# Kernel tuning notes

Hardware: AMD Instinct MI355X
Metric: run time of the kernel (lower is better)

## Reference

```python
import jax, jax.numpy as jnp
import numpy as np


def setup_inputs() -> dict:
    key = jax.random.key(0)
    kq, kk, kv = jax.random.split(key, 3)
    B, L, S, H, E = 2, 2048, 2048, 8, 64
    queries = jax.random.normal(kq, (B, L, H, E), dtype=jnp.float32)
    keys = jax.random.normal(kk, (B, S, H, E), dtype=jnp.float32)
    values = jax.random.normal(kv, (B, S, H, E), dtype=jnp.float32)
    a1 = jnp.float32(1.0)
    a2 = jnp.float32(1.0)
    return {"queries": queries, "keys": keys, "values": values, "a1": a1, "a2": a2}


def reference(queries, keys, values, a1, a2):
    # queries: (B,L,H,E); keys/values: (B,S,H,E)
    E = queries.shape[-1]
    scale = 1.0 / jnp.sqrt(jnp.float32(E))
    # shared QK scores: (B,H,L,S)
    qk = jnp.einsum('blhe,bshe->bhls', queries, keys) * scale
    # sparse branch: relu^2 (dropout = identity in eval)
    ssa = jnp.square(jax.nn.relu(qk))
    ssa_out = jnp.einsum('bhls,bshd->blhd', ssa, values)
    # dense branch: softmax over keys
    dsa = jax.nn.softmax(qk, axis=-1)
    dsa_out = jnp.einsum('bhls,bshd->blhd', dsa, values)
    w1 = jnp.exp(a1)
    w2 = jnp.exp(a2)
    alpha1 = w1 / (w1 + w2)
    alpha2 = w2 / (w1 + w2)
    return alpha1 * ssa_out + alpha2 * dsa_out
```

## Files before the change

kernel.cpp:

```cpp
#include <hip/hip_runtime.h>

typedef short short4v __attribute__((ext_vector_type(4)));
typedef short short8v __attribute__((ext_vector_type(8)));
typedef float float4v __attribute__((ext_vector_type(4)));
typedef unsigned short u16;

#define NB 2
#define NL 2048
#define NS 2048
#define NH 8
#define NE 64
#define HE (NH*NE)
#define NLT (NL/64)
#define NST (NS/64)
#define TILE_U16 4096

static __device__ __forceinline__ unsigned pk2bf(float a, float b) {
  union { float f; unsigned u; } x, y; x.f = a; y.f = b;
  return __builtin_amdgcn_perm(y.u + 0x8000u, x.u + 0x8000u, 0x07060302u);
}

static __device__ __forceinline__ unsigned cvtpk(float a, float b) {
  unsigned r;
  asm("v_cvt_pk_bf16_f32 %0, %1, %2" : "=v"(r) : "v"(a), "v"(b));
  return r;
}

static __device__ __forceinline__ float fexp2(float x) {
  float r;
  asm("v_exp_f32 %0, %1" : "=v"(r) : "v"(x));
  return r;
}

#define GLD16(gp, lp) __builtin_amdgcn_global_load_lds( \
    (const __attribute__((address_space(1))) void*)(gp), \
    (__attribute__((address_space(3))) void*)(lp), 16, 0, 0)

static __device__ __forceinline__ int fK(int s) { return (s & 3) | ((s >> 1) & 4); }

__global__ __launch_bounds__(256)
void prepack(const float* __restrict__ kp, const float* __restrict__ vp,
             u16* __restrict__ kimg, u16* __restrict__ vimg)
{
  __shared__ __align__(16) u16 ldsv[TILE_U16];

  const int bid  = blockIdx.x;
  const int tile = bid >> 1;
  const int doV  = bid & 1;
  const int st = tile & (NST - 1);
  const int bh = tile >> 5;
  const int h  = bh & (NH - 1);
  const int b  = bh >> 3;
  const int s0 = st * 64;
  const size_t base = (size_t)b * NS * HE + h * NE;
  const int tid  = threadIdx.x;
  const int wv   = tid >> 6;
  const int lane = tid & 63;
  const int ln7  = lane & 7;

  if (!doV) {
    u16* kt = kimg + (size_t)tile * TILE_U16;
    for (int slot = tid; slot < 512; slot += 256) {
      const int srow = slot >> 3, p = slot & 7, c = p ^ fK(srow);
      const float* src = kp + base + (size_t)(s0 + srow) * HE + c * 8;
      float4 x0 = *(const float4*)src;
      float4 x1 = *(const float4*)(src + 4);
      unsigned d[4] = { pk2bf(x0.x, x0.y), pk2bf(x0.z, x0.w),
                        pk2bf(x1.x, x1.y), pk2bf(x1.z, x1.w) };
      *(int4*)(kt + slot * 8) = *(const int4*)d;
    }
    return;
  }

  u16* vt = vimg + (size_t)tile * TILE_U16;
  {
    const float* vcol = vp + base + (size_t)(s0 + wv * 16) * HE + lane;
    unsigned vr[8];
    #pragma unroll
    for (int jj = 0; jj < 8; ++jj)
      vr[jj] = pk2bf(vcol[(size_t)(2 * jj) * HE], vcol[(size_t)(2 * jj + 1) * HE]);
    #pragma unroll
    for (int i = 0; i < 2; ++i) {
      const int cs = (2 * wv + i) ^ ln7;
      int4 t4 = make_int4((int)vr[4*i+0], (int)vr[4*i+1],
                          (int)vr[4*i+2], (int)vr[4*i+3]);
      *(int4*)(&ldsv[lane * 64 + cs * 8]) = t4;
    }
  }
  __syncthreads();
  {
    const int4* s = (const int4*)ldsv;
    int4* dst = (int4*)vt;
    dst[tid]       = s[tid];
    dst[tid + 256] = s[tid + 256];
  }
}

__global__ __launch_bounds__(512, 2)
void assa_fwd(const float* __restrict__ qp, const u16* __restrict__ kimg,
              const u16* __restrict__ vimg, const float* __restrict__ a1p,
              const float* __restrict__ a2p, float* __restrict__ op)
{
  __shared__ __align__(16) u16 ldsb[2][2][2 * TILE_U16];

  const int tid  = threadIdx.x;
  const int wv   = tid >> 6;
  const int ws   = wv & 3;
  const int strm = wv >> 2;
  const int lane = tid & 63;
  const int ln15 = lane & 15;
  const int ln7  = lane & 7;
  const int quad = lane >> 4;

  const int bid = blockIdx.x;
  const int bh  = bid & 15;
  const int lt  = bid >> 4;
  const int h   = bh & (NH - 1);
  const int b   = bh >> 3;

  const int lbase = lt * 64 + ws * 16;

  short8v qf0, qf1;
  {
    const float qs = 0.125f * 1.44269504089f;
    const float* qrow = qp + ((size_t)(b * NL + lbase + ln15)) * HE + h * NE + quad * 8;
    float4 q0 = *(const float4*)(qrow);
    float4 q1 = *(const float4*)(qrow + 4);
    float4 q2 = *(const float4*)(qrow + 32);
    float4 q3 = *(const float4*)(qrow + 36);
    unsigned d0[4] = { pk2bf(qs*q0.x, qs*q0.y), pk2bf(qs*q0.z, qs*q0.w),
                       pk2bf(qs*q1.x, qs*q1.y), pk2bf(qs*q1.z, qs*q1.w) };
    unsigned d1[4] = { pk2bf(qs*q2.x, qs*q2.y), pk2bf(qs*q2.z, qs*q2.w),
                       pk2bf(qs*q3.x, qs*q3.y), pk2bf(qs*q3.z, qs*q3.w) };
    qf0 = *(const short8v*)d0;
    qf1 = *(const short8v*)d1;
  }

  short8v ones8;
  #pragma unroll
  for (int j = 0; j < 8; ++j) ones8[j] = (short)0x3F80;

  const size_t tbase = (size_t)bh * NST;

  float4v acc_s[4], acc_d[4], acc_l;
  #pragma unroll
  for (int t = 0; t < 4; ++t)
    #pragma unroll
    for (int r = 0; r < 4; ++r) { acc_s[t][r] = 0.0f; acc_d[t][r] = 0.0f; }
  #pragma unroll
  for (int r = 0; r < 4; ++r) acc_l[r] = 0.0f;

  auto dma_tile = [&](int st, int nb) {
    const int hf = ws & 1;
    const u16* g;
    u16* l;
    if (ws < 2) {
      g = kimg + (tbase + st) * TILE_U16 + hf * 2048 + lane * 8;
      l = &ldsb[strm][nb][hf * 2048];
    } else {
      g = vimg + (tbase + st) * TILE_U16 + hf * 2048 + lane * 8;
      l = &ldsb[strm][nb][TILE_U16 + hf * 2048];
    }
    GLD16(g,        l);
    GLD16(g +  512, l +  512);
    GLD16(g + 1024, l + 1024);
    GLD16(g + 1536, l + 1536);
  };

  dma_tile(strm, 0);

  const int rperm = 8 * (ln15 >> 2) + (ln15 & 3);
  const int fk    = (ln15 & 3) | (((ln15 >> 2) & 1) << 2);

  for (int it = 0; it < NST / 2; ++it) {
    asm volatile("s_waitcnt vmcnt(0)" ::: "memory");
    __builtin_amdgcn_s_barrier();
    asm volatile("" ::: "memory");
    if (it + 1 < NST / 2) dma_tile(2 * (it + 1) + strm, (it + 1) & 1);

    const u16* kb_l = ldsb[strm][it & 1];
    const u16* vb_l = kb_l + TILE_U16;

    #pragma unroll
    for (int U = 0; U < 2; ++U) {
      float4v sa0, sa1;
      #pragma unroll
      for (int r = 0; r < 4; ++r) { sa0[r] = 0.0f; sa1[r] = 0.0f; }
      const u16* krow0 = &kb_l[(32 * U + rperm) * 64];
      const u16* krow1 = krow0 + 4 * 64;
      short8v kf00 = *(const short8v*)(krow0 + (quad ^ fk) * 8);
      short8v kf01 = *(const short8v*)(krow0 + ((4 + quad) ^ fk) * 8);
      short8v kf10 = *(const short8v*)(krow1 + (quad ^ fk) * 8);
      short8v kf11 = *(const short8v*)(krow1 + ((4 + quad) ^ fk) * 8);
      __builtin_amdgcn_s_setprio(1);
      sa0 = __builtin_amdgcn_mfma_f32_16x16x32_bf16(kf00, qf0, sa0, 0, 0, 0);
      sa0 = __builtin_amdgcn_mfma_f32_16x16x32_bf16(kf01, qf1, sa0, 0, 0, 0);
      sa1 = __builtin_amdgcn_mfma_f32_16x16x32_bf16(kf10, qf0, sa1, 0, 0, 0);
      sa1 = __builtin_amdgcn_mfma_f32_16x16x32_bf16(kf11, qf1, sa1, 0, 0, 0);
      __builtin_amdgcn_s_setprio(0);

      float ps[8], pd[8];
      #pragma unroll
      for (int r = 0; r < 4; ++r) {
        float s0 = sa0[r], s1 = sa1[r];
        float r0 = s0 > 0.0f ? s0 : 0.0f;
        float r1 = s1 > 0.0f ? s1 : 0.0f;
        ps[r] = r0 * r0;  ps[4 + r] = r1 * r1;
        pd[r] = fexp2(s0); pd[4 + r] = fexp2(s1);
      }
      unsigned da[4] = { cvtpk(ps[0], ps[1]), cvtpk(ps[2], ps[3]),
                         cvtpk(ps[4], ps[5]), cvtpk(ps[6], ps[7]) };
      unsigned db[4] = { cvtpk(pd[0], pd[1]), cvtpk(pd[2], pd[3]),
                         cvtpk(pd[4], pd[5]), cvtpk(pd[6], pd[7]) };
      short8v as8 = *(const short8v*)da;
      short8v ad8 = *(const short8v*)db;

      __builtin_amdgcn_s_setprio(1);
      acc_l = __builtin_amdgcn_mfma_f32_16x16x32_bf16(ad8, ones8, acc_l, 0, 0, 0);

      #pragma unroll
      for (int t = 0; t < 4; ++t) {
        short8v vf = *(const short8v*)(&vb_l[(t * 16 + ln15) * 64 +
                        (((4 * U + quad) ^ ln7) * 8)]);
        acc_s[t] = __builtin_amdgcn_mfma_f32_16x16x32_bf16(as8, vf, acc_s[t], 0, 0, 0);
        acc_d[t] = __builtin_amdgcn_mfma_f32_16x16x32_bf16(ad8, vf, acc_d[t], 0, 0, 0);
      }
      __builtin_amdgcn_s_setprio(0);
    }
  }

  __syncthreads();
  float* red = (float*)&ldsb[0][0][0];
  const int idx = ws * 64 + lane;
  if (strm == 1) {
    #pragma unroll
    for (int t = 0; t < 4; ++t)
      #pragma unroll
      for (int r = 0; r < 4; ++r) {
        red[(t * 4 + r) * 256 + idx]        = acc_s[t][r];
        red[(16 + t * 4 + r) * 256 + idx]   = acc_d[t][r];
      }
    #pragma unroll
    for (int r = 0; r < 4; ++r)
      red[(32 + r) * 256 + idx] = acc_l[r];
  }
  __syncthreads();
  if (strm == 0) {
    #pragma unroll
    for (int t = 0; t < 4; ++t)
      #pragma unroll
      for (int r = 0; r < 4; ++r) {
        acc_s[t][r] += red[(t * 4 + r) * 256 + idx];
        acc_d[t][r] += red[(16 + t * 4 + r) * 256 + idx];
      }
    #pragma unroll
    for (int r = 0; r < 4; ++r)
      acc_l[r] += red[(32 + r) * 256 + idx];

    const float w1 = __expf(a1p[0]), w2 = __expf(a2p[0]);
    const float al1 = (w1 / (w1 + w2)) * 0.48045301391820142f;
    const float al2 = w2 / (w1 + w2);

    float c_d[4];
    #pragma unroll
    for (int r = 0; r < 4; ++r) c_d[r] = al2 / acc_l[r];

    #pragma unroll
    for (int t = 0; t < 4; ++t) {
      #pragma unroll
      for (int r = 0; r < 4; ++r) {
        float val = al1 * acc_s[t][r] + c_d[r] * acc_d[t][r];
        const int l = lbase + quad * 4 + r;
        const int e = t * 16 + ln15;
        op[((size_t)(b * NL + l)) * HE + h * NE + e] = val;
      }
    }
  }
}

extern "C" void kernel_launch(void* const* d_in, const int* in_sizes, int n_in,
                              void* d_out, int out_size, void* d_ws, size_t ws_size,
                              hipStream_t stream) {
  const float* q  = (const float*)d_in[0];
  const float* k  = (const float*)d_in[1];
  const float* v  = (const float*)d_in[2];
  const float* a1 = (const float*)d_in[3];
  const float* a2 = (const float*)d_in[4];
  float* out = (float*)d_out;
  (void)in_sizes; (void)n_in; (void)out_size; (void)ws_size;

  u16* kimg = (u16*)d_ws;
  u16* vimg = kimg + (size_t)NB * NH * NST * TILE_U16;

  prepack<<<dim3(NB * NH * NST * 2), dim3(256), 0, stream>>>(k, v, kimg, vimg);
  assa_fwd<<<dim3(NB * NH * NLT), dim3(512), 0, stream>>>(q, kimg, vimg, a1, a2, out);
}
```

Measured before the change: 107.9 us.

## Fuse K/V bf16 prepack into attention kernel with per-head atomic barrier

Removes the separate prepack launch. Each attention block first converts one K/V tile to bf16 in the workspace, then signals a per-(batch,head) counter. It spin-waits until all 32 tiles for that head are ready before running the main loop. This saves one kernel launch and the gap between launches, but adds a memset, the spin-wait, and a risk of deadlock if not all blocks are co-resident (512 blocks at 2 per CU).

Result: slower. 204.4 us (+89.4%).

```diff
diff --git a/kernel.cpp b/kernel.cpp
--- a/kernel.cpp
+++ b/kernel.cpp
@@ -38,68 +38,12 @@
 
 static __device__ __forceinline__ int fK(int s) { return (s & 3) | ((s >> 1) & 4); }
 
-__global__ __launch_bounds__(256)
-void prepack(const float* __restrict__ kp, const float* __restrict__ vp,
-             u16* __restrict__ kimg, u16* __restrict__ vimg)
-{
-  __shared__ __align__(16) u16 ldsv[TILE_U16];
-
-  const int bid  = blockIdx.x;
-  const int tile = bid >> 1;
-  const int doV  = bid & 1;
-  const int st = tile & (NST - 1);
-  const int bh = tile >> 5;
-  const int h  = bh & (NH - 1);
-  const int b  = bh >> 3;
-  const int s0 = st * 64;
-  const size_t base = (size_t)b * NS * HE + h * NE;
-  const int tid  = threadIdx.x;
-  const int wv   = tid >> 6;
-  const int lane = tid & 63;
-  const int ln7  = lane & 7;
-
-  if (!doV) {
-    u16* kt = kimg + (size_t)tile * TILE_U16;
-    for (int slot = tid; slot < 512; slot += 256) {
-      const int srow = slot >> 3, p = slot & 7, c = p ^ fK(srow);
-      const float* src = kp + base + (size_t)(s0 + srow) * HE + c * 8;
-      float4 x0 = *(const float4*)src;
-      float4 x1 = *(const float4*)(src + 4);
-      unsigned d[4] = { pk2bf(x0.x, x0.y), pk2bf(x0.z, x0.w),
-                        pk2bf(x1.x, x1.y), pk2bf(x1.z, x1.w) };
-      *(int4*)(kt + slot * 8) = *(const int4*)d;
-    }
-    return;
-  }
-
-  u16* vt = vimg + (size_t)tile * TILE_U16;
-  {
-    const float* vcol = vp + base + (size_t)(s0 + wv * 16) * HE + lane;
-    unsigned vr[8];
-    #pragma unroll
-    for (int jj = 0; jj < 8; ++jj)
-      vr[jj] = pk2bf(vcol[(size_t)(2 * jj) * HE], vcol[(size_t)(2 * jj + 1) * HE]);
-    #pragma unroll
-    for (int i = 0; i < 2; ++i) {
-      const int cs = (2 * wv + i) ^ ln7;
-      int4 t4 = make_int4((int)vr[4*i+0], (int)vr[4*i+1],
-                          (int)vr[4*i+2], (int)vr[4*i+3]);
-      *(int4*)(&ldsv[lane * 64 + cs * 8]) = t4;
-    }
-  }
-  __syncthreads();
-  {
-    const int4* s = (const int4*)ldsv;
-    int4* dst = (int4*)vt;
-    dst[tid]       = s[tid];
-    dst[tid + 256] = s[tid + 256];
-  }
-}
-
 __global__ __launch_bounds__(512, 2)
-void assa_fwd(const float* __restrict__ qp, const u16* __restrict__ kimg,
-              const u16* __restrict__ vimg, const float* __restrict__ a1p,
-              const float* __restrict__ a2p, float* __restrict__ op)
+void assa_fused(const float* __restrict__ qp, const float* __restrict__ kp,
+                const float* __restrict__ vp, const float* __restrict__ a1p,
+                const float* __restrict__ a2p, float* __restrict__ op,
+                u16* __restrict__ kimg, u16* __restrict__ vimg,
+                unsigned* __restrict__ cnt)
 {
   __shared__ __align__(16) u16 ldsb[2][2][2 * TILE_U16];
 
@@ -117,6 +61,54 @@
   const int lt  = bid >> 4;
   const int h   = bh & (NH - 1);
   const int b   = bh >> 3;
+
+  {
+    const int pst = lt;
+    const int s0  = pst * 64;
+    const size_t pbase = (size_t)b * NS * HE + h * NE;
+    const int ptile = bh * NST + pst;
+
+    if (tid < 256) {
+      u16* kt = kimg + (size_t)ptile * TILE_U16;
+      for (int slot = tid; slot < 512; slot += 256) {
+        const int srow = slot >> 3, p = slot & 7, c = p ^ fK(srow);
+        const float* src = kp + pbase + (size_t)(s0 + srow) * HE + c * 8;
+        float4 x0 = *(const float4*)src;
+        float4 x1 = *(const float4*)(src + 4);
+        unsigned d[4] = { pk2bf(x0.x, x0.y), pk2bf(x0.z, x0.w),
+                          pk2bf(x1.x, x1.y), pk2bf(x1.z, x1.w) };
+        *(int4*)(kt + slot * 8) = *(const int4*)d;
+      }
+    } else {
+      const int wv2 = wv - 4;
+      u16* ldsv = &ldsb[0][0][0];
+      const float* vcol = vp + pbase + (size_t)(s0 + wv2 * 16) * HE + lane;
+      unsigned vr[8];
+      #pragma unroll
+      for (int jj = 0; jj < 8; ++jj)
+        vr[jj] = pk2bf(vcol[(size_t)(2 * jj) * HE], vcol[(size_t)(2 * jj + 1) * HE]);
+      #pragma unroll
+      for (int i = 0; i < 2; ++i) {
+        const int cs = (2 * wv2 + i) ^ ln7;
+        int4 t4 = make_int4((int)vr[4*i+0], (int)vr[4*i+1],
+                            (int)vr[4*i+2], (int)vr[4*i+3]);
+        *(int4*)(&ldsv[lane * 64 + cs * 8]) = t4;
+      }
+    }
+    __syncthreads();
+    if (tid >= 256) {
+      const int tid2 = tid - 256;
+      const int4* s = (const int4*)&ldsb[0][0][0];
+      int4* dst = (int4*)(vimg + (size_t)ptile * TILE_U16);
+      dst[tid2]       = s[tid2];
+      dst[tid2 + 256] = s[tid2 + 256];
+    }
+    __syncthreads();
+    if (tid == 0) {
+      __threadfence();
+      atomicAdd(&cnt[bh], 1u);
+    }
+  }
 
   const int lbase = lt * 64 + ws * 16;
 
@@ -136,6 +128,13 @@
     qf1 = *(const short8v*)d1;
   }
 
+  if (tid == 0) {
+    while (atomicAdd(&cnt[bh], 0u) < 32u) __builtin_amdgcn_s_sleep(16);
+  }
+  __syncthreads();
+  if (lane == 0) __threadfence();
+  __syncthreads();
+
   short8v ones8;
   #pragma unroll
   for (int j = 0; j < 8; ++j) ones8[j] = (short)0x3F80;
@@ -291,7 +290,9 @@
 
   u16* kimg = (u16*)d_ws;
   u16* vimg = kimg + (size_t)NB * NH * NST * TILE_U16;
-
-  prepack<<<dim3(NB * NH * NST * 2), dim3(256), 0, stream>>>(k, v, kimg, vimg);
-  assa_fwd<<<dim3(NB * NH * NLT), dim3(512), 0, stream>>>(q, kimg, vimg, a1, a2, out);
-}
+  unsigned* cnt = (unsigned*)((char*)d_ws + (size_t)16 * 1024 * 1024);
+
+  hipMemsetAsync(cnt, 0, 16 * sizeof(unsigned), stream);
+  assa_fused<<<dim3(NB * NH * NLT), dim3(512), 0, stream>>>(
+      q, k, v, a1, a2, out, kimg, vimg, cnt);
+}
```
